# Optimization experiments

Measured on AMD Instinct MI355X. Metric: run time of the kernel, lower is better.

Reference implementation:

```python
import jax, jax.numpy as jnp
import numpy as np

B, S, D, O, E, K = 4, 8192, 1024, 1024, 4, 2

def setup_inputs() -> dict:
    key = jax.random.key(0)
    k1, k2, k3, k4, k5 = jax.random.split(key, 5)
    x = jax.random.normal(k1, (B, S, D), dtype=jnp.float32)
    expert_weights = jax.random.uniform(k2, (B, S, K), dtype=jnp.float32)
    top_k_indices = jax.random.randint(k3, (B, S, K), 0, E).astype(jnp.int64)
    # per-expert linear params: nn.Linear(unified_dim, output_dim) for each expert
    W = jax.random.normal(k4, (E, D, O), dtype=jnp.float32) * (1.0 / np.sqrt(D))
    b = jax.random.normal(k5, (E, O), dtype=jnp.float32) * 0.01
    return {"x": x, "expert_weights": expert_weights, "top_k_indices": top_k_indices, "W": W, "b": b}

def reference(x, expert_weights, top_k_indices, W, b):
    # Dense compute of all experts, as the torch module does: [B,S,E,O]
    expert_outputs = jnp.einsum('bsd,edo->bseo', x, W) + b  # broadcast bias [E,O]
    # Gather top-k expert outputs per token: idx [B,S,K] -> [B,S,K,O]
    gathered = jnp.take_along_axis(expert_outputs, top_k_indices[..., None].astype(jnp.int32), axis=2)
    # Weighted combine over k
    output = jnp.sum(expert_weights[..., None] * gathered, axis=2)  # [B,S,O]
    return output
```

## Files before the change

kernel.cpp:

```cpp
#include <hip/hip_runtime.h>
#include <hip/hip_bf16.h>
#include <stdint.h>

#define M_TOK 32768
#define DIM   1024
#define ODIM  1024
#define NEXP  4
#define KTOT  4096
#define NBIN  16
#define MTILES 272
#define PERM_LEN (MTILES * 128)
#define GEMM_GRID (8 * 34 * 16)

#define NB_CVTX 4096
#define NB_CVTW 4096
#define NB_HIST 128
#define NB_PRE  (NB_CVTX + NB_CVTW + NB_HIST)

typedef unsigned short u16;
typedef __bf16 bf16x8 __attribute__((ext_vector_type(8)));
typedef float  f32x4  __attribute__((ext_vector_type(4)));

__device__ inline u16 f2bf(float f) {
  union { float f; unsigned u; } v; v.f = f;
  unsigned u = v.u;
  unsigned r = u + 0x7FFFu + ((u >> 16) & 1u);
  return (u16)(r >> 16);
}

__device__ inline unsigned pack2(float lo, float hi) {
  return (unsigned)f2bf(lo) | ((unsigned)f2bf(hi) << 16);
}

__device__ inline void async16(const void* g, void* l) {
  __builtin_amdgcn_global_load_lds(
      (const __attribute__((address_space(1))) unsigned int*)g,
      (__attribute__((address_space(3))) unsigned int*)l, 16, 0, 0);
}

__global__ void pre_pass(const float* __restrict__ x, uint4* __restrict__ xb,
                         const float* __restrict__ W, u16* __restrict__ Wt,
                         const int* __restrict__ tki, int* __restrict__ ctrl) {
  __shared__ float t[32][33];
  __shared__ int h[NBIN];
  const int b = blockIdx.x, tid = threadIdx.x;

  if (b < NB_CVTX) {
    const float4* xv = (const float4*)x;
    const int n8 = M_TOK * DIM / 8;
    for (int i = b * 256 + tid; i < n8; i += NB_CVTX * 256) {
      float4 a = xv[2 * i];
      float4 c = xv[2 * i + 1];
      uint4 o;
      o.x = pack2(a.x, a.y); o.y = pack2(a.z, a.w);
      o.z = pack2(c.x, c.y); o.w = pack2(c.z, c.w);
      xb[i] = o;
    }
  } else if (b < NB_CVTX + NB_CVTW) {
    const int bb = b - NB_CVTX;
    const int kk0 = (bb & 127) * 32, n0 = (bb >> 7) * 32;
    const int tx = tid & 31, ty = tid >> 5;
#pragma unroll
    for (int j = 0; j < 32; j += 8)
      t[ty + j][tx] = W[(size_t)(kk0 + ty + j) * ODIM + n0 + tx];
    __syncthreads();
#pragma unroll
    for (int j = 0; j < 32; j += 8)
      Wt[(size_t)(n0 + ty + j) * KTOT + kk0 + tx] = f2bf(t[tx][ty + j]);
  } else {
    const int bb = b - NB_CVTX - NB_CVTW;
    if (tid < NBIN) h[tid] = 0;
    __syncthreads();
    int tok = bb * 256 + tid;
    int e0 = tki[2 * tok] & 3, e1 = tki[2 * tok + 1] & 3;
    atomicAdd(&h[e0 * 4 + e1], 1);
    __syncthreads();
    if (tid < NBIN) atomicAdd(&ctrl[tid], h[tid]);
  }
}

__global__ void scatter(const int* __restrict__ tki, const float* __restrict__ ew,
                        int* __restrict__ ctrl,
                        int* __restrict__ perm, float2* __restrict__ wgt2) {
  __shared__ int h[NBIN], gbase[NBIN], cur[NBIN], offs[NBIN];
  int tid = threadIdx.x;
  if (tid < NBIN) { h[tid] = 0; cur[tid] = 0; }
  if (tid == 0) {
    int off = 0;
#pragma unroll
    for (int b = 0; b < NBIN; ++b) {
      offs[b] = off;
      off += (ctrl[b] + 127) & ~127;
    }
  }
  __syncthreads();
  int t = blockIdx.x * 256 + tid;
  int e0 = tki[2 * t] & 3, e1 = tki[2 * t + 1] & 3;
  int bin = e0 * 4 + e1;
  atomicAdd(&h[bin], 1);
  __syncthreads();
  if (tid < NBIN && h[tid] > 0)
    gbase[tid] = offs[tid] + atomicAdd(&ctrl[16 + tid], h[tid]);
  __syncthreads();
  int rank = atomicAdd(&cur[bin], 1);
  int pos = gbase[bin] + rank;
  perm[pos] = t;
  float2 w; w.x = ew[2 * t]; w.y = ew[2 * t + 1];
  wgt2[pos] = w;
}

__global__ __launch_bounds__(256, 4) void moe_gemm(
    const u16* __restrict__ Xb,
    const u16* __restrict__ Wt,
    const int* __restrict__ perm,
    const float2* __restrict__ wgt2,
    const int* __restrict__ tki,
    const float* __restrict__ bias,
    float* __restrict__ out)
{
  __shared__ __align__(16) u16 As [128 * 64];
  __shared__ __align__(16) u16 Bs0[64 * 64];
  __shared__ __align__(16) u16 Bs1[64 * 64];
  __shared__ int    rowsS[128];
  __shared__ float2 wgtS[128];

  const int d = blockIdx.x;
  const int slot = d >> 3;
  const int mtile = (d & 7) * (MTILES / 8) + (slot >> 4);
  const int nblk = slot & 15;
  const int base = mtile * 128;
  const int t0 = perm[base];
  if (t0 < 0) return;
  const int e0 = tki[2 * t0] & 3, e1 = tki[2 * t0 + 1] & 3;

  const int tid = threadIdx.x;
  if (tid < 128) { rowsS[tid] = perm[base + tid]; wgtS[tid] = wgt2[base + tid]; }

  const int wid = tid >> 6, lane = tid & 63;
  const int bcol = nblk * 64;
  const int wr = wid >> 1, wc = wid & 1;
  const int fcol = bcol + wc * 32;

  f32x4 acc0[4][2], acc1[4][2];
#pragma unroll
  for (int m = 0; m < 4; ++m)
#pragma unroll
    for (int n = 0; n < 2; ++n) {
      acc0[m][n] = (f32x4){0.f, 0.f, 0.f, 0.f};
      acc1[m][n] = (f32x4){0.f, 0.f, 0.f, 0.f};
    }

  const int srow = lane >> 3;
  const int scol = ((lane & 7) ^ srow) * 8;
  const int hi16 = (lane >> 4) * 16;
  const int swz  = (lane & 7) << 4;
  const char* AsB  = (const char*)As;
  const char* Bs0B = (const char*)Bs0;
  const char* Bs1B = (const char*)Bs1;

  __syncthreads();

  const u16* aptr[4];
  const u16* b0ptr[2];
  const u16* b1ptr[2];
#pragma unroll
  for (int i = 0; i < 4; ++i) {
    int c = wid * 4 + i;
    int r = rowsS[c * 8 + srow];
    if (r < 0) r = 0;
    aptr[i] = Xb + (size_t)r * DIM + scol;
  }
#pragma unroll
  for (int i = 0; i < 2; ++i) {
    int c = wid * 2 + i;
    size_t wrow = (size_t)(bcol + c * 8 + srow) * KTOT + scol;
    b0ptr[i] = Wt + wrow + e0 * DIM;
    b1ptr[i] = Wt + wrow + e1 * DIM;
  }

  for (int kt = 0; kt < DIM / 64; ++kt) {
    __syncthreads();
#pragma unroll
    for (int i = 0; i < 4; ++i)
      async16(aptr[i] + kt * 64, &As[(wid * 4 + i) * 512]);
#pragma unroll
    for (int i = 0; i < 2; ++i) {
      async16(b0ptr[i] + kt * 64, &Bs0[(wid * 2 + i) * 512]);
      async16(b1ptr[i] + kt * 64, &Bs1[(wid * 2 + i) * 512]);
    }
    __syncthreads();
#pragma unroll
    for (int kk = 0; kk < 2; ++kk) {
      const int cb = (kk * 64 + hi16) ^ swz;
      bf16x8 af[4], bf0[2], bf1[2];
#pragma unroll
      for (int m = 0; m < 4; ++m) {
        int row = wr * 64 + m * 16 + (lane & 15);
        af[m] = *reinterpret_cast<const bf16x8*>(AsB + row * 128 + cb);
      }
#pragma unroll
      for (int n = 0; n < 2; ++n) {
        int row = wc * 32 + n * 16 + (lane & 15);
        bf0[n] = *reinterpret_cast<const bf16x8*>(Bs0B + row * 128 + cb);
        bf1[n] = *reinterpret_cast<const bf16x8*>(Bs1B + row * 128 + cb);
      }
#pragma unroll
      for (int m = 0; m < 4; ++m)
#pragma unroll
        for (int n = 0; n < 2; ++n) {
          acc0[m][n] = __builtin_amdgcn_mfma_f32_16x16x32_bf16(af[m], bf0[n], acc0[m][n], 0, 0, 0);
          acc1[m][n] = __builtin_amdgcn_mfma_f32_16x16x32_bf16(af[m], bf1[n], acc1[m][n], 0, 0, 0);
        }
    }
  }

  float bb0[2], bb1[2];
#pragma unroll
  for (int n = 0; n < 2; ++n) {
    int col = fcol + n * 16 + (lane & 15);
    bb0[n] = bias[e0 * ODIM + col];
    bb1[n] = bias[e1 * ODIM + col];
  }

#pragma unroll
  for (int m = 0; m < 4; ++m) {
#pragma unroll
    for (int r = 0; r < 4; ++r) {
      int rl = wr * 64 + m * 16 + (lane >> 4) * 4 + r;
      int t = rowsS[rl];
      if (t < 0) continue;
      float2 w = wgtS[rl];
      size_t o = (size_t)t * ODIM + fcol + (lane & 15);
#pragma unroll
      for (int n = 0; n < 2; ++n)
        out[o + n * 16] = w.x * (acc0[m][n][r] + bb0[n]) + w.y * (acc1[m][n][r] + bb1[n]);
    }
  }
}

extern "C" void kernel_launch(void* const* d_in, const int* in_sizes, int n_in,
                              void* d_out, int out_size, void* d_ws, size_t ws_size,
                              hipStream_t stream) {
  const float* x    = (const float*)d_in[0];
  const float* ew   = (const float*)d_in[1];
  const int*   tki  = (const int*)d_in[2];
  const float* W    = (const float*)d_in[3];
  const float* bias = (const float*)d_in[4];
  float* out = (float*)d_out;

  char* ws = (char*)d_ws;
  u16*    xb   = (u16*)ws;
  u16*    wt   = (u16*)(ws + 67108864);
  int*    ctrl = (int*)(ws + 75497472);
  int*    perm = (int*)(ws + 75497728);
  float2* wgt2 = (float2*)(ws + 75636992);

  hipMemsetAsync(ctrl, 0, 128, stream);
  hipMemsetAsync(perm, 0xFF, PERM_LEN * sizeof(int), stream);
  pre_pass<<<NB_PRE, 256, 0, stream>>>(x, (uint4*)xb, W, wt, tki, ctrl);
  scatter<<<128, 256, 0, stream>>>(tki, ew, ctrl, perm, wgt2);
  moe_gemm<<<GEMM_GRID, 256, 0, stream>>>(xb, wt, perm, wgt2, tki, bias, out);
}
```

Before: 190.0 us.

## Fuse fp32-to-bf16 conversion of x into GEMM with register-prefetched double buffering

Removes the separate pass that converted x to bf16 in workspace. The GEMM now loads fp32 activations directly into registers, converts them with v_cvt_pk_bf16_f32 and writes them to LDS, while B tiles are double-buffered and prefetched one k-step ahead. This saves the full write and re-read of a bf16 copy of x. In exchange each GEMM block reads fp32 x, twice the bytes, and x is re-read once per 64-wide N block (16 times), not from a compact bf16 copy. Higher register use also lowers the occupancy target to 3.

Result: slower. 230.0 us (+21.1%).

```diff
diff --git a/kernel.cpp b/kernel.cpp
--- a/kernel.cpp
+++ b/kernel.cpp
@@ -5,21 +5,21 @@
 #define M_TOK 32768
 #define DIM   1024
 #define ODIM  1024
-#define NEXP  4
 #define KTOT  4096
 #define NBIN  16
 #define MTILES 272
 #define PERM_LEN (MTILES * 128)
 #define GEMM_GRID (8 * 34 * 16)
-
-#define NB_CVTX 4096
+#define NT (DIM / 64)
+
 #define NB_CVTW 4096
 #define NB_HIST 128
-#define NB_PRE  (NB_CVTX + NB_CVTW + NB_HIST)
+#define NB_PRE  (NB_CVTW + NB_HIST)
 
 typedef unsigned short u16;
 typedef __bf16 bf16x8 __attribute__((ext_vector_type(8)));
 typedef float  f32x4  __attribute__((ext_vector_type(4)));
+typedef unsigned int u32x4 __attribute__((ext_vector_type(4)));
 
 __device__ inline u16 f2bf(float f) {
   union { float f; unsigned u; } v; v.f = f;
@@ -28,37 +28,20 @@
   return (u16)(r >> 16);
 }
 
-__device__ inline unsigned pack2(float lo, float hi) {
-  return (unsigned)f2bf(lo) | ((unsigned)f2bf(hi) << 16);
-}
-
 __device__ inline void async16(const void* g, void* l) {
   __builtin_amdgcn_global_load_lds(
       (const __attribute__((address_space(1))) unsigned int*)g,
       (__attribute__((address_space(3))) unsigned int*)l, 16, 0, 0);
 }
 
-__global__ void pre_pass(const float* __restrict__ x, uint4* __restrict__ xb,
-                         const float* __restrict__ W, u16* __restrict__ Wt,
+__global__ void pre_pass(const float* __restrict__ W, u16* __restrict__ Wt,
                          const int* __restrict__ tki, int* __restrict__ ctrl) {
   __shared__ float t[32][33];
   __shared__ int h[NBIN];
   const int b = blockIdx.x, tid = threadIdx.x;
 
-  if (b < NB_CVTX) {
-    const float4* xv = (const float4*)x;
-    const int n8 = M_TOK * DIM / 8;
-    for (int i = b * 256 + tid; i < n8; i += NB_CVTX * 256) {
-      float4 a = xv[2 * i];
-      float4 c = xv[2 * i + 1];
-      uint4 o;
-      o.x = pack2(a.x, a.y); o.y = pack2(a.z, a.w);
-      o.z = pack2(c.x, c.y); o.w = pack2(c.z, c.w);
-      xb[i] = o;
-    }
-  } else if (b < NB_CVTX + NB_CVTW) {
-    const int bb = b - NB_CVTX;
-    const int kk0 = (bb & 127) * 32, n0 = (bb >> 7) * 32;
+  if (b < NB_CVTW) {
+    const int kk0 = (b & 127) * 32, n0 = (b >> 7) * 32;
     const int tx = tid & 31, ty = tid >> 5;
 #pragma unroll
     for (int j = 0; j < 32; j += 8)
@@ -68,7 +51,7 @@
     for (int j = 0; j < 32; j += 8)
       Wt[(size_t)(n0 + ty + j) * KTOT + kk0 + tx] = f2bf(t[tx][ty + j]);
   } else {
-    const int bb = b - NB_CVTX - NB_CVTW;
+    const int bb = b - NB_CVTW;
     if (tid < NBIN) h[tid] = 0;
     __syncthreads();
     int tok = bb * 256 + tid;
@@ -109,8 +92,8 @@
   wgt2[pos] = w;
 }
 
-__global__ __launch_bounds__(256, 4) void moe_gemm(
-    const u16* __restrict__ Xb,
+__global__ __launch_bounds__(256, 3) void moe_gemm(
+    const float* __restrict__ X,
     const u16* __restrict__ Wt,
     const int* __restrict__ perm,
     const float2* __restrict__ wgt2,
@@ -118,9 +101,8 @@
     const float* __restrict__ bias,
     float* __restrict__ out)
 {
-  __shared__ __align__(16) u16 As [128 * 64];
-  __shared__ __align__(16) u16 Bs0[64 * 64];
-  __shared__ __align__(16) u16 Bs1[64 * 64];
+  __shared__ __align__(16) u16 As[128 * 64];
+  __shared__ __align__(16) u16 Bs[2][2][64 * 64];
   __shared__ int    rowsS[128];
   __shared__ float2 wgtS[128];
 
@@ -151,25 +133,23 @@
     }
 
   const int srow = lane >> 3;
-  const int scol = ((lane & 7) ^ srow) * 8;
+  const int lcol = lane & 7;
+  const int scol = (lcol ^ srow) * 8;
   const int hi16 = (lane >> 4) * 16;
   const int swz  = (lane & 7) << 4;
-  const char* AsB  = (const char*)As;
-  const char* Bs0B = (const char*)Bs0;
-  const char* Bs1B = (const char*)Bs1;
-
-  __syncthreads();
-
-  const u16* aptr[4];
-  const u16* b0ptr[2];
-  const u16* b1ptr[2];
+
+  __syncthreads();
+
+  const float* aptrF[4];
 #pragma unroll
   for (int i = 0; i < 4; ++i) {
     int c = wid * 4 + i;
     int r = rowsS[c * 8 + srow];
     if (r < 0) r = 0;
-    aptr[i] = Xb + (size_t)r * DIM + scol;
-  }
+    aptrF[i] = X + (size_t)r * DIM + lcol * 8;
+  }
+  const u16* b0ptr[2];
+  const u16* b1ptr[2];
 #pragma unroll
   for (int i = 0; i < 2; ++i) {
     int c = wid * 2 + i;
@@ -177,18 +157,41 @@
     b0ptr[i] = Wt + wrow + e0 * DIM;
     b1ptr[i] = Wt + wrow + e1 * DIM;
   }
-
-  for (int kt = 0; kt < DIM / 64; ++kt) {
-    __syncthreads();
-#pragma unroll
-    for (int i = 0; i < 4; ++i)
-      async16(aptr[i] + kt * 64, &As[(wid * 4 + i) * 512]);
-#pragma unroll
-    for (int i = 0; i < 2; ++i) {
-      async16(b0ptr[i] + kt * 64, &Bs0[(wid * 2 + i) * 512]);
-      async16(b1ptr[i] + kt * 64, &Bs1[(wid * 2 + i) * 512]);
-    }
-    __syncthreads();
+  char* awr = (char*)As + (size_t)(wid * 4) * 1024 + srow * 128 + ((lcol ^ srow) << 4);
+
+  float4 aLo[4], aHi[4];
+#define A_LOAD(kt) do { _Pragma("unroll")                                   \
+    for (int i_ = 0; i_ < 4; ++i_) {                                        \
+      const float4* p_ = (const float4*)(aptrF[i_] + (kt) * 64);            \
+      aLo[i_] = p_[0]; aHi[i_] = p_[1]; } } while (0)
+#define B_STAGE(bb, kt) do { _Pragma("unroll")                              \
+    for (int i_ = 0; i_ < 2; ++i_) {                                        \
+      async16(b0ptr[i_] + (kt) * 64, &Bs[bb][0][(wid * 2 + i_) * 512]);     \
+      async16(b1ptr[i_] + (kt) * 64, &Bs[bb][1][(wid * 2 + i_) * 512]); } } while (0)
+#define A_CVT_WRITE() do { _Pragma("unroll")                                \
+    for (int i_ = 0; i_ < 4; ++i_) {                                        \
+      unsigned w0_, w1_, w2_, w3_;                                          \
+      asm volatile("v_cvt_pk_bf16_f32 %0, %1, %2" : "=v"(w0_) : "v"(aLo[i_].x), "v"(aLo[i_].y)); \
+      asm volatile("v_cvt_pk_bf16_f32 %0, %1, %2" : "=v"(w1_) : "v"(aLo[i_].z), "v"(aLo[i_].w)); \
+      asm volatile("v_cvt_pk_bf16_f32 %0, %1, %2" : "=v"(w2_) : "v"(aHi[i_].x), "v"(aHi[i_].y)); \
+      asm volatile("v_cvt_pk_bf16_f32 %0, %1, %2" : "=v"(w3_) : "v"(aHi[i_].z), "v"(aHi[i_].w)); \
+      u32x4 v_ = {w0_, w1_, w2_, w3_};                                      \
+      *(u32x4*)(awr + i_ * 1024) = v_; } } while (0)
+
+  A_LOAD(0);
+  B_STAGE(0, 0);
+  A_CVT_WRITE();
+  __syncthreads();
+
+  for (int kt = 0; kt < NT; ++kt) {
+    const int b = kt & 1;
+    if (kt + 1 < NT) {
+      A_LOAD(kt + 1);
+      B_STAGE(b ^ 1, kt + 1);
+    }
+    const char* AsB  = (const char*)As;
+    const char* Bs0B = (const char*)Bs[b][0];
+    const char* Bs1B = (const char*)Bs[b][1];
 #pragma unroll
     for (int kk = 0; kk < 2; ++kk) {
       const int cb = (kk * 64 + hi16) ^ swz;
@@ -212,7 +215,13 @@
           acc1[m][n] = __builtin_amdgcn_mfma_f32_16x16x32_bf16(af[m], bf1[n], acc1[m][n], 0, 0, 0);
         }
     }
-  }
+    __syncthreads();
+    if (kt + 1 < NT) A_CVT_WRITE();
+    __syncthreads();
+  }
+#undef A_LOAD
+#undef B_STAGE
+#undef A_CVT_WRITE
 
   float bb0[2], bb1[2];
 #pragma unroll
@@ -249,15 +258,14 @@
   float* out = (float*)d_out;
 
   char* ws = (char*)d_ws;
-  u16*    xb   = (u16*)ws;
-  u16*    wt   = (u16*)(ws + 67108864);
-  int*    ctrl = (int*)(ws + 75497472);
-  int*    perm = (int*)(ws + 75497728);
-  float2* wgt2 = (float2*)(ws + 75636992);
+  u16*    wt   = (u16*)ws;
+  int*    ctrl = (int*)(ws + 8388608);
+  int*    perm = (int*)(ws + 8388864);
+  float2* wgt2 = (float2*)(ws + 8528128);
 
   hipMemsetAsync(ctrl, 0, 128, stream);
   hipMemsetAsync(perm, 0xFF, PERM_LEN * sizeof(int), stream);
-  pre_pass<<<NB_PRE, 256, 0, stream>>>(x, (uint4*)xb, W, wt, tki, ctrl);
+  pre_pass<<<NB_PRE, 256, 0, stream>>>(W, wt, tki, ctrl);
   scatter<<<128, 256, 0, stream>>>(tki, ew, ctrl, perm, wgt2);
-  moe_gemm<<<GEMM_GRID, 256, 0, stream>>>(xb, wt, perm, wgt2, tki, bias, out);
-}
+  moe_gemm<<<GEMM_GRID, 256, 0, stream>>>(x, wt, perm, wgt2, tki, bias, out);
+}
```
